# Kernel optimization log

Hardware: AMD Instinct MI355X
Metric: run time of the kernel (lower is better)

The kernel has to match this reference:

```python
import jax, jax.numpy as jnp
import numpy as np

B, QL, T, H = 32, 1, 2048, 512


def setup_inputs() -> dict:
    key = jax.random.key(0)
    ks = jax.random.split(key, 10)
    n = lambda i, shape, sc=1.0: jax.random.normal(ks[i], shape, dtype=jnp.float32) * sc
    inv = 1.0 / np.sqrt(H)
    return {
        "query": n(0, (B, QL, H)),
        "value": n(1, (B, T, H)),
        "last_attn": jax.random.uniform(ks[2], (B, T), dtype=jnp.float32),
        "conv_w": n(3, (H, 1, 3), 0.1),   # Conv1d weight (out_ch, in_ch=1, k=3)
        "conv_b": n(4, (H,), 0.1),
        "q_w": n(5, (H, H), inv),          # query_proj (no bias)
        "v_w": n(6, (H, H), inv),          # value_proj (no bias)
        "s_w": n(7, (1, H), inv),          # score_proj weight
        "s_b": n(8, (1,), 0.1),            # score_proj bias
        "bias": n(9, (H,), 0.1),           # learned additive bias
    }


def reference(query, value, last_attn, conv_w, conv_b, q_w, v_w, s_w, s_b, bias):
    Tlen = last_attn.shape[1]
    # Conv1d(in=1, out=H, k=3, pad=1) over last_attn, then transpose -> (B, T, H)
    pad = jnp.pad(last_attn, ((0, 0), (1, 1)))
    frames = jnp.stack([pad[:, k:k + Tlen] for k in range(3)], axis=0)  # (3, B, T)
    conv_attn = jnp.einsum('hk,kbt->bth', conv_w[:, 0, :], frames) + conv_b  # (B, T, H)
    q = jnp.einsum('bqh,oh->bqo', query, q_w)   # (B, 1, H)
    v = jnp.einsum('bth,oh->bto', value, v_w)   # (B, T, H)
    e = jnp.tanh(q + v + conv_attn + bias)      # (B, T, H), q broadcasts over T
    score = jnp.einsum('bth,oh->bt', e, s_w) + s_b  # (B, T)
    # smoothing=True branch: sigmoid then L1-normalize
    score = jax.nn.sigmoid(score)
    attn = score / jnp.sum(score, axis=-1, keepdims=True)
    context = jnp.einsum('bt,bth->bh', attn, value)  # bmm(attn[:,None,:], value).squeeze(1)
    return context, attn
```

## Files before the change

### kernel.cpp

```cpp
#include <hip/hip_runtime.h>
#include <math.h>

#define B 32
#define T 2048
#define H 512

#define BT2 64
#define APAD 40

typedef __attribute__((ext_vector_type(8))) __bf16 bf16x8;
typedef __attribute__((ext_vector_type(4))) __bf16 bf16x4v;
typedef __attribute__((ext_vector_type(4))) float f32x4;
typedef __attribute__((ext_vector_type(4))) float floatx4;

union pack8 { bf16x4v h; uint2 u; };

static __device__ __forceinline__ void gl_lds16(const void* g, void* l) {
    __builtin_amdgcn_global_load_lds(
        (const __attribute__((address_space(1))) void*)g,
        (__attribute__((address_space(3))) void*)l, 16, 0, 0);
}

__global__ __launch_bounds__(256) void k_init(const float* __restrict__ query,
                                              const float* __restrict__ q_w,
                                              const float* __restrict__ bias,
                                              const float* __restrict__ v_w,
                                              float* __restrict__ qpb,
                                              unsigned short* __restrict__ wbf,
                                              float* __restrict__ ctx_num,
                                              float* __restrict__ denom) {
    const int blk = blockIdx.x;
    const int tid = threadIdx.x;

    if (blk >= 288) {
#pragma unroll
        for (int i = 0; i < 16; ++i) {
            const int off = tid * 4 + i * 1024;
            *(f32x4*)(ctx_num + off) = (f32x4){0.f, 0.f, 0.f, 0.f};
        }
        if (tid < B) denom[tid] = 0.f;
        return;
    }
    if (blk >= 256) {
        const int c = blk - 256;
        const size_t base = (size_t)c * 8192 + tid * 4;
#pragma unroll
        for (int i = 0; i < 8; ++i) {
            const size_t off = base + (size_t)i * 1024;
            f32x4 a = *(const f32x4*)(v_w + off);
            pack8 p;
            p.h = __builtin_convertvector(a, bf16x4v);
            *(uint2*)(wbf + off) = p.u;
        }
        return;
    }

    const int b = blk >> 3;
    const int s = blk & 7;
    const int wave = tid >> 6;
    const int lane = tid & 63;

    const float* qb = query + (size_t)b * H + lane * 8;
    float4 q0 = *(const float4*)qb;
    float4 q1 = *(const float4*)(qb + 4);

    const int o0 = s * 64 + wave * 16;
#pragma unroll
    for (int i = 0; i < 16; ++i) {
        const int o = o0 + i;
        const float* wr = q_w + (size_t)o * H + lane * 8;
        float4 w0 = *(const float4*)wr;
        float4 w1 = *(const float4*)(wr + 4);
        float acc = w0.x * q0.x + w0.y * q0.y + w0.z * q0.z + w0.w * q0.w +
                    w1.x * q1.x + w1.y * q1.y + w1.z * q1.z + w1.w * q1.w;
#pragma unroll
        for (int m = 1; m < 64; m <<= 1) acc += __shfl_xor(acc, m);
        if (lane == 0) qpb[b * H + o] = acc + bias[o];
    }
}

__global__ __launch_bounds__(512, 4) void k2_fused(const float* __restrict__ value,
                                                   const unsigned short* __restrict__ wbf,
                                                   const float* __restrict__ la,
                                                   const float* __restrict__ conv_w,
                                                   const float* __restrict__ conv_b,
                                                   const float* __restrict__ s_w,
                                                   const float* __restrict__ qpb,
                                                   const float* __restrict__ s_b,
                                                   float* __restrict__ pre_sg,
                                                   float* __restrict__ ctx_num,
                                                   float* __restrict__ denom) {
    __shared__ __align__(16) unsigned short As[BT2 * APAD];
    __shared__ __align__(16) unsigned short Bs[H * 32];
    __shared__ float las[BT2 + 2];
    __shared__ float redp[BT2][9];
    __shared__ float sgs[BT2];

    const int t0 = blockIdx.x * BT2;
    const int b  = blockIdx.y;
    const int tid = threadIdx.x;
    const int wave = tid >> 6;
    const int lane = tid & 63;
    const int tx   = lane & 15;
    const int quad = lane >> 4;
    const int wn   = wave * 64;

    if (tid < BT2 + 2) {
        const int t = t0 + tid - 1;
        las[tid] = (t >= 0 && t < T) ? la[b * T + t] : 0.f;
    }

    float qp4[4], sw4[4], cb4[4], c04[4], c14[4], c24[4];
#pragma unroll
    for (int ni = 0; ni < 4; ++ni) {
        const int ol = wn + ni * 16 + tx;
        qp4[ni] = qpb[b * H + ol];
        sw4[ni] = s_w[ol];
        cb4[ni] = conv_b[ol];
        c04[ni] = conv_w[ol * 3 + 0];
        c14[ni] = conv_w[ol * 3 + 1];
        c24[ni] = conv_w[ol * 3 + 2];
    }

    floatx4 acc[4][4];
#pragma unroll
    for (int i = 0; i < 4; ++i)
#pragma unroll
        for (int j = 0; j < 4; ++j) acc[i][j] = (floatx4){0.f, 0.f, 0.f, 0.f};

    const int arow = tid >> 3;
    const int acol = (tid & 7) * 4;
    const float* agp = value + ((size_t)b * T + t0 + arow) * H + acol;
    const int brow = lane >> 2;
    const int bcol = (lane & 3) * 8;
    const unsigned short* gB[4];
    unsigned short* lB[4];
#pragma unroll
    for (int c = 0; c < 4; ++c) {
        const int chunk = wave + c * 8;
        gB[c] = wbf + (size_t)(chunk * 16 + brow) * H + bcol;
        lB[c] = &Bs[chunk * 512];
    }

    for (int kc = 0; kc < H; kc += 32) {
        f32x4 av = *(const f32x4*)(agp + kc);

        __syncthreads();
#pragma unroll
        for (int c = 0; c < 4; ++c) gl_lds16(gB[c] + kc, lB[c]);

        pack8 p;
        p.h = __builtin_convertvector(av, bf16x4v);
        *(uint2*)&As[arow * APAD + acol] = p.u;

        __syncthreads();

        bf16x8 af[4], bfr[4];
#pragma unroll
        for (int mi = 0; mi < 4; ++mi)
            af[mi] = *(const bf16x8*)&As[(mi * 16 + tx) * APAD + quad * 8];
#pragma unroll
        for (int ni = 0; ni < 4; ++ni)
            bfr[ni] = *(const bf16x8*)&Bs[(wn + ni * 16 + tx) * 32 + quad * 8];
#pragma unroll
        for (int mi = 0; mi < 4; ++mi)
#pragma unroll
            for (int ni = 0; ni < 4; ++ni)
                acc[mi][ni] = __builtin_amdgcn_mfma_f32_16x16x32_bf16(
                    af[mi], bfr[ni], acc[mi][ni], 0, 0, 0);
    }

    float sacc[16];
#pragma unroll
    for (int i = 0; i < 16; ++i) sacc[i] = 0.f;
#pragma unroll
    for (int ni = 0; ni < 4; ++ni) {
#pragma unroll
        for (int mi = 0; mi < 4; ++mi)
#pragma unroll
            for (int r = 0; r < 4; ++r) {
                const int tl = mi * 16 + quad * 4 + r;
                const float conv = c04[ni] * las[tl] + c14[ni] * las[tl + 1] +
                                   c24[ni] * las[tl + 2] + cb4[ni];
                const float x = acc[mi][ni][r] + qp4[ni] + conv;
                const float ex = __expf(2.f * x);
                const float th = 1.f - 2.f * __builtin_amdgcn_rcpf(ex + 1.f);
                sacc[mi * 4 + r] += sw4[ni] * th;
            }
    }
#pragma unroll
    for (int i = 0; i < 16; ++i) {
        float v = sacc[i];
        v += __shfl_xor(v, 1);
        v += __shfl_xor(v, 2);
        v += __shfl_xor(v, 4);
        v += __shfl_xor(v, 8);
        if (tx == 0) redp[(i >> 2) * 16 + quad * 4 + (i & 3)][wave] = v;
    }
    __syncthreads();

    if (tid < BT2) {
        float sc = s_b[0];
#pragma unroll
        for (int w = 0; w < 8; ++w) sc += redp[tid][w];
        const float sg = 1.f / (1.f + __expf(-sc));
        sgs[tid] = sg;
        pre_sg[b * T + t0 + tid] = sg;
        float dsum = sg;
#pragma unroll
        for (int m = 1; m < 64; m <<= 1) dsum += __shfl_xor(dsum, m);
        if (tid == 0) atomicAdd(&denom[b], dsum);
    }
    __syncthreads();

    float* redc = (float*)Bs;
    const int h4 = (tid & 127) * 4;
    const int tp = tid >> 7;
    f32x4 a = {0.f, 0.f, 0.f, 0.f};
    const float* vb = value + ((size_t)b * T + t0) * H + h4;
    for (int t = tp; t < BT2; t += 4) {
        const float w = sgs[t];
        f32x4 v = *(const f32x4*)(vb + (size_t)t * H);
        a.x += w * v.x; a.y += w * v.y; a.z += w * v.z; a.w += w * v.w;
    }
    *(f32x4*)&redc[tp * 512 + h4] = a;
    __syncthreads();
    if (tid < 128) {
        const int h = tid * 4;
        f32x4 r0 = *(const f32x4*)&redc[0 * 512 + h];
        f32x4 r1 = *(const f32x4*)&redc[1 * 512 + h];
        f32x4 r2 = *(const f32x4*)&redc[2 * 512 + h];
        f32x4 r3 = *(const f32x4*)&redc[3 * 512 + h];
        atomicAdd(&ctx_num[b * H + h + 0], r0.x + r1.x + r2.x + r3.x);
        atomicAdd(&ctx_num[b * H + h + 1], r0.y + r1.y + r2.y + r3.y);
        atomicAdd(&ctx_num[b * H + h + 2], r0.z + r1.z + r2.z + r3.z);
        atomicAdd(&ctx_num[b * H + h + 3], r0.w + r1.w + r2.w + r3.w);
    }
}

__global__ __launch_bounds__(256) void k3_scale(const float* __restrict__ pre_sg,
                                                const float* __restrict__ ctx_num,
                                                const float* __restrict__ denom,
                                                float* __restrict__ attn_out,
                                                float* __restrict__ ctx) {
    const int b = blockIdx.x;
    const int tid = threadIdx.x;
    const float inv = 1.f / denom[b];
#pragma unroll
    for (int i = 0; i < 8; ++i) {
        const int t = tid + i * 256;
        attn_out[b * T + t] = pre_sg[b * T + t] * inv;
    }
#pragma unroll
    for (int i = 0; i < 2; ++i) {
        const int h = tid + i * 256;
        ctx[b * H + h] = ctx_num[b * H + h] * inv;
    }
}

extern "C" void kernel_launch(void* const* d_in, const int* in_sizes, int n_in,
                              void* d_out, int out_size, void* d_ws, size_t ws_size,
                              hipStream_t stream) {
    const float* query  = (const float*)d_in[0];
    const float* value  = (const float*)d_in[1];
    const float* la     = (const float*)d_in[2];
    const float* conv_w = (const float*)d_in[3];
    const float* conv_b = (const float*)d_in[4];
    const float* q_w    = (const float*)d_in[5];
    const float* v_w    = (const float*)d_in[6];
    const float* s_w    = (const float*)d_in[7];
    const float* s_b    = (const float*)d_in[8];
    const float* bias   = (const float*)d_in[9];

    float* out  = (float*)d_out;
    float* ctx  = out;
    float* attn = out + B * H;

    float* qpb     = (float*)d_ws;
    float* pre_sg  = qpb + B * H;
    float* ctx_num = pre_sg + B * T;
    float* denom   = ctx_num + B * H;
    unsigned short* wbf = (unsigned short*)(denom + 64);

    k_init<<<289, 256, 0, stream>>>(query, q_w, bias, v_w, qpb, wbf, ctx_num, denom);

    dim3 g2(T / BT2, B);
    k2_fused<<<g2, 512, 0, stream>>>(value, wbf, la, conv_w, conv_b, s_w, qpb, s_b,
                                     pre_sg, ctx_num, denom);

    k3_scale<<<B, 256, 0, stream>>>(pre_sg, ctx_num, denom, attn, ctx);
}
```

Baseline: 280.3 us.

## Load GEMM fragments directly from global into registers with prefetch, dropping LDS staging

The fused score kernel no longer stages value and weight tiles through shared memory. Each lane now loads its MFMA fragments straight from global memory into registers, converting to bf16 in registers, and prefetches the next k-chunk one step ahead. This removes the two barriers per k-step and the LDS traffic. In exchange, each of the 8 waves reloads the same value rows (8x redundant global/L2 reads of A), register pressure rises, and launch bounds drop from 4 to 2 blocks per CU.

After: 394.1 us. 1.41x slower.

```diff
diff --git a/kernel.cpp b/kernel.cpp
--- a/kernel.cpp
+++ b/kernel.cpp
@@ -6,7 +6,6 @@
 #define H 512
 
 #define BT2 64
-#define APAD 40
 
 typedef __attribute__((ext_vector_type(8))) __bf16 bf16x8;
 typedef __attribute__((ext_vector_type(4))) __bf16 bf16x4v;
@@ -14,12 +13,7 @@
 typedef __attribute__((ext_vector_type(4))) float floatx4;
 
 union pack8 { bf16x4v h; uint2 u; };
-
-static __device__ __forceinline__ void gl_lds16(const void* g, void* l) {
-    __builtin_amdgcn_global_load_lds(
-        (const __attribute__((address_space(1))) void*)g,
-        (__attribute__((address_space(3))) void*)l, 16, 0, 0);
-}
+union fragU { bf16x4v q[2]; bf16x8 v; };
 
 __global__ __launch_bounds__(256) void k_init(const float* __restrict__ query,
                                               const float* __restrict__ q_w,
@@ -79,22 +73,21 @@
     }
 }
 
-__global__ __launch_bounds__(512, 4) void k2_fused(const float* __restrict__ value,
-                                                   const unsigned short* __restrict__ wbf,
-                                                   const float* __restrict__ la,
-                                                   const float* __restrict__ conv_w,
-                                                   const float* __restrict__ conv_b,
-                                                   const float* __restrict__ s_w,
-                                                   const float* __restrict__ qpb,
-                                                   const float* __restrict__ s_b,
-                                                   float* __restrict__ pre_sg,
-                                                   float* __restrict__ ctx_num,
-                                                   float* __restrict__ denom) {
-    __shared__ __align__(16) unsigned short As[BT2 * APAD];
-    __shared__ __align__(16) unsigned short Bs[H * 32];
+__global__ __launch_bounds__(512, 2) void k2_reg(const float* __restrict__ value,
+                                                 const unsigned short* __restrict__ wbf,
+                                                 const float* __restrict__ la,
+                                                 const float* __restrict__ conv_w,
+                                                 const float* __restrict__ conv_b,
+                                                 const float* __restrict__ s_w,
+                                                 const float* __restrict__ qpb,
+                                                 const float* __restrict__ s_b,
+                                                 float* __restrict__ pre_sg,
+                                                 float* __restrict__ ctx_num,
+                                                 float* __restrict__ denom) {
     __shared__ float las[BT2 + 2];
     __shared__ float redp[BT2][9];
     __shared__ float sgs[BT2];
+    __shared__ float redc[4 * H];
 
     const int t0 = blockIdx.x * BT2;
     const int b  = blockIdx.y;
@@ -110,6 +103,63 @@
         las[tid] = (t >= 0 && t < T) ? la[b * T + t] : 0.f;
     }
 
+    floatx4 acc[4][4];
+#pragma unroll
+    for (int i = 0; i < 4; ++i)
+#pragma unroll
+        for (int j = 0; j < 4; ++j) acc[i][j] = (floatx4){0.f, 0.f, 0.f, 0.f};
+
+    const float* aB = value + ((size_t)b * T + t0 + tx) * H + quad * 8;
+    const unsigned short* bB = wbf + (size_t)(wn + tx) * H + quad * 8;
+
+    f32x4 alo[4], ahi[4];
+    bf16x8 bfr[4];
+#pragma unroll
+    for (int mi = 0; mi < 4; ++mi) {
+        const float* p = aB + (size_t)mi * 16 * H;
+        alo[mi] = *(const f32x4*)p;
+        ahi[mi] = *(const f32x4*)(p + 4);
+    }
+#pragma unroll
+    for (int ni = 0; ni < 4; ++ni)
+        bfr[ni] = *(const bf16x8*)(bB + (size_t)ni * 16 * H);
+
+    for (int kc = 0; kc < H; kc += 32) {
+        f32x4 nlo[4], nhi[4];
+        bf16x8 nbf[4];
+        if (kc + 32 < H) {
+#pragma unroll
+            for (int mi = 0; mi < 4; ++mi) {
+                const float* p = aB + (size_t)mi * 16 * H + kc + 32;
+                nlo[mi] = *(const f32x4*)p;
+                nhi[mi] = *(const f32x4*)(p + 4);
+            }
+#pragma unroll
+            for (int ni = 0; ni < 4; ++ni)
+                nbf[ni] = *(const bf16x8*)(bB + (size_t)ni * 16 * H + kc + 32);
+        }
+
+        bf16x8 af[4];
+#pragma unroll
+        for (int mi = 0; mi < 4; ++mi) {
+            fragU u;
+            u.q[0] = __builtin_convertvector(alo[mi], bf16x4v);
+            u.q[1] = __builtin_convertvector(ahi[mi], bf16x4v);
+            af[mi] = u.v;
+        }
+#pragma unroll
+        for (int mi = 0; mi < 4; ++mi)
+#pragma unroll
+            for (int ni = 0; ni < 4; ++ni)
+                acc[mi][ni] = __builtin_amdgcn_mfma_f32_16x16x32_bf16(
+                    af[mi], bfr[ni], acc[mi][ni], 0, 0, 0);
+
+#pragma unroll
+        for (int mi = 0; mi < 4; ++mi) { alo[mi] = nlo[mi]; ahi[mi] = nhi[mi]; }
+#pragma unroll
+        for (int ni = 0; ni < 4; ++ni) bfr[ni] = nbf[ni];
+    }
+
     float qp4[4], sw4[4], cb4[4], c04[4], c14[4], c24[4];
 #pragma unroll
     for (int ni = 0; ni < 4; ++ni) {
@@ -120,54 +170,6 @@
         c04[ni] = conv_w[ol * 3 + 0];
         c14[ni] = conv_w[ol * 3 + 1];
         c24[ni] = conv_w[ol * 3 + 2];
-    }
-
-    floatx4 acc[4][4];
-#pragma unroll
-    for (int i = 0; i < 4; ++i)
-#pragma unroll
-        for (int j = 0; j < 4; ++j) acc[i][j] = (floatx4){0.f, 0.f, 0.f, 0.f};
-
-    const int arow = tid >> 3;
-    const int acol = (tid & 7) * 4;
-    const float* agp = value + ((size_t)b * T + t0 + arow) * H + acol;
-    const int brow = lane >> 2;
-    const int bcol = (lane & 3) * 8;
-    const unsigned short* gB[4];
-    unsigned short* lB[4];
-#pragma unroll
-    for (int c = 0; c < 4; ++c) {
-        const int chunk = wave + c * 8;
-        gB[c] = wbf + (size_t)(chunk * 16 + brow) * H + bcol;
-        lB[c] = &Bs[chunk * 512];
-    }
-
-    for (int kc = 0; kc < H; kc += 32) {
-        f32x4 av = *(const f32x4*)(agp + kc);
-
-        __syncthreads();
-#pragma unroll
-        for (int c = 0; c < 4; ++c) gl_lds16(gB[c] + kc, lB[c]);
-
-        pack8 p;
-        p.h = __builtin_convertvector(av, bf16x4v);
-        *(uint2*)&As[arow * APAD + acol] = p.u;
-
-        __syncthreads();
-
-        bf16x8 af[4], bfr[4];
-#pragma unroll
-        for (int mi = 0; mi < 4; ++mi)
-            af[mi] = *(const bf16x8*)&As[(mi * 16 + tx) * APAD + quad * 8];
-#pragma unroll
-        for (int ni = 0; ni < 4; ++ni)
-            bfr[ni] = *(const bf16x8*)&Bs[(wn + ni * 16 + tx) * 32 + quad * 8];
-#pragma unroll
-        for (int mi = 0; mi < 4; ++mi)
-#pragma unroll
-            for (int ni = 0; ni < 4; ++ni)
-                acc[mi][ni] = __builtin_amdgcn_mfma_f32_16x16x32_bf16(
-                    af[mi], bfr[ni], acc[mi][ni], 0, 0, 0);
     }
 
     float sacc[16];
@@ -213,7 +215,6 @@
     }
     __syncthreads();
 
-    float* redc = (float*)Bs;
     const int h4 = (tid & 127) * 4;
     const int tp = tid >> 7;
     f32x4 a = {0.f, 0.f, 0.f, 0.f};
@@ -223,14 +224,14 @@
         f32x4 v = *(const f32x4*)(vb + (size_t)t * H);
         a.x += w * v.x; a.y += w * v.y; a.z += w * v.z; a.w += w * v.w;
     }
-    *(f32x4*)&redc[tp * 512 + h4] = a;
+    *(f32x4*)&redc[tp * H + h4] = a;
     __syncthreads();
     if (tid < 128) {
         const int h = tid * 4;
-        f32x4 r0 = *(const f32x4*)&redc[0 * 512 + h];
-        f32x4 r1 = *(const f32x4*)&redc[1 * 512 + h];
-        f32x4 r2 = *(const f32x4*)&redc[2 * 512 + h];
-        f32x4 r3 = *(const f32x4*)&redc[3 * 512 + h];
+        f32x4 r0 = *(const f32x4*)&redc[0 * H + h];
+        f32x4 r1 = *(const f32x4*)&redc[1 * H + h];
+        f32x4 r2 = *(const f32x4*)&redc[2 * H + h];
+        f32x4 r3 = *(const f32x4*)&redc[3 * H + h];
         atomicAdd(&ctx_num[b * H + h + 0], r0.x + r1.x + r2.x + r3.x);
         atomicAdd(&ctx_num[b * H + h + 1], r0.y + r1.y + r2.y + r3.y);
         atomicAdd(&ctx_num[b * H + h + 2], r0.z + r1.z + r2.z + r3.z);
@@ -285,8 +286,8 @@
     k_init<<<289, 256, 0, stream>>>(query, q_w, bias, v_w, qpb, wbf, ctx_num, denom);
 
     dim3 g2(T / BT2, B);
-    k2_fused<<<g2, 512, 0, stream>>>(value, wbf, la, conv_w, conv_b, s_w, qpb, s_b,
-                                     pre_sg, ctx_num, denom);
+    k2_reg<<<g2, 512, 0, stream>>>(value, wbf, la, conv_w, conv_b, s_w, qpb, s_b,
+                                   pre_sg, ctx_num, denom);
 
     k3_scale<<<B, 256, 0, stream>>>(pre_sg, ctx_num, denom, attn, ctx);
 }
```
